# Performance work log

Hardware: AMD Instinct MI355X
Metric: run time of the kernel (lower is better)

## Reference

```python
import jax, jax.numpy as jnp
import numpy as np

B, N_ANG, LX, LY, LZ = 2, 120, 128, 128, 128


def _rotate_z(vol, phi):
    """Rotate vol [B,Lx,Ly,Lz] by phi radians (counterclockwise) in the (x,y)
    plane about the grid center, bilinear interpolation, zero padding.
    Mirrors pytomography's rotate_detector_z (bilinear grid-sample rotate)."""
    Lx, Ly = vol.shape[1], vol.shape[2]
    dt = vol.dtype
    cx = (Lx - 1) / 2.0
    cy = (Ly - 1) / 2.0
    xs = jnp.arange(Lx, dtype=dt) - cx
    ys = jnp.arange(Ly, dtype=dt) - cy
    X, Y = jnp.meshgrid(xs, ys, indexing="ij")  # [Lx,Ly]
    c, s = jnp.cos(phi), jnp.sin(phi)
    # inverse rotation maps each output pixel to its source location
    sx = c * X + s * Y + cx
    sy = -s * X + c * Y + cy
    x0 = jnp.floor(sx)
    y0 = jnp.floor(sy)
    wx = (sx - x0)[None, :, :, None]
    wy = (sy - y0)[None, :, :, None]
    x0i = x0.astype(jnp.int32)
    y0i = y0.astype(jnp.int32)

    def gather(xi, yi):
        valid = (xi >= 0) & (xi < Lx) & (yi >= 0) & (yi < Ly)
        xic = jnp.clip(xi, 0, Lx - 1)
        yic = jnp.clip(yi, 0, Ly - 1)
        v = vol[:, xic, yic, :]  # [B,Lx,Ly,Lz]
        return v * valid.astype(dt)[None, :, :, None]

    v00 = gather(x0i, y0i)
    v01 = gather(x0i, y0i + 1)
    v10 = gather(x0i + 1, y0i)
    v11 = gather(x0i + 1, y0i + 1)
    return (v00 * (1 - wx) * (1 - wy) + v01 * (1 - wx) * wy
            + v10 * wx * (1 - wy) + v11 * wx * wy)


def setup_inputs() -> dict:
    key = jax.random.key(0)
    image = jax.random.uniform(key, (B, N_ANG, LY, LZ), dtype=jnp.float32)
    angles = jnp.linspace(0.0, 360.0, N_ANG, endpoint=False).astype(jnp.float32)
    return {"image": image, "angles": angles}


def reference(image, angles, delta=1e-11):
    # image: [B, N_angles, Lr, Lz]; angles in degrees.
    Bn, Na, Lr, Lz = image.shape
    Lx = Ly = Lr
    dt = image.dtype
    phis = -jnp.deg2rad(angles).astype(dt)  # negative=True -> back-rotation

    def step(carry, inp):
        obj_acc, norm_acc = carry
        proj, phi = inp  # proj: [B, Lr, Lz]
        # image[:, i].unsqueeze(1) * ones([B, Lx, Ly, Lz]): broadcast along x
        obj_i = jnp.broadcast_to(proj[:, None, :, :], (Bn, Lx, Ly, Lz))
        norm_i = jnp.ones((Bn, Lx, Ly, Lz), dt)
        obj_acc = obj_acc + _rotate_z(obj_i, phi)
        norm_acc = norm_acc + _rotate_z(norm_i, phi)
        return (obj_acc, norm_acc), None

    init = (jnp.zeros((Bn, Lx, Ly, Lz), dt), jnp.zeros((Bn, Lx, Ly, Lz), dt))
    (obj, norm), _ = jax.lax.scan(step, init, (jnp.swapaxes(image, 0, 1), phis))
    return obj / (norm + jnp.asarray(delta, dt))
```

## Files before the change

kernel.cpp:

```cpp
#include <hip/hip_runtime.h>

namespace {

constexpr int L     = 128;
constexpr int NANG  = 120;
constexpr size_t H16_BYTES = (size_t)2 * NANG * L * L * 2;

typedef __fp16 f16x2 __attribute__((ext_vector_type(2)));
typedef __fp16 f16x4 __attribute__((ext_vector_type(4)));
typedef float  f32x4 __attribute__((ext_vector_type(4)));

__global__ __launch_bounds__(256) void cvt16_kernel(const float* __restrict__ in,
                                                    unsigned* __restrict__ out) {
    const int i = ((int)blockIdx.x * 256 + (int)threadIdx.x) * 4;
    const float4 v = *reinterpret_cast<const float4*>(in + i);
    f16x2 a = __builtin_amdgcn_cvt_pkrtz(v.x, v.y);
    f16x2 b = __builtin_amdgcn_cvt_pkrtz(v.z, v.w);
    uint2 st;
    st.x = *reinterpret_cast<unsigned*>(&a);
    st.y = *reinterpret_cast<unsigned*>(&b);
    *reinterpret_cast<uint2*>(out + i / 2) = st;
}

template <bool F16>
__global__ __launch_bounds__(1024, 4) void bp_kernel(
    const void* __restrict__ imgv,
    const float* __restrict__ angles,
    float* __restrict__ out)
{
    constexpr unsigned SLICE = F16 ? 32768u : 65536u;
    constexpr unsigned ROWB  = F16 ? 256u  : 512u;
    constexpr int      RSH   = F16 ? 8 : 9;

    __shared__ uint4    wtab[NANG * 64];
    __shared__ float2   acs[NANG];
    __shared__ unsigned arloB[NANG];
    __shared__ alignas(16) float nrmtab[64];

    const int tid = threadIdx.x;
    const int bid = (int)blockIdx.x;
    const int n   = ((bid & 7) << 5) | (bid >> 3);
    int xt = 0, yt = 0;
#pragma unroll
    for (int i = 0; i < 4; ++i) {
        xt |= ((n >> (2 * i)) & 1) << i;
        yt |= ((n >> (2 * i + 1)) & 1) << i;
    }
    const int xb = xt * 8, yb = yt * 8;
    const float cx = (L - 1) * 0.5f;

    if (tid < NANG) {
        const float phi = -angles[tid] * 0.017453292519943295f;
        float s, c;
        sincosf(phi, &s, &c);
        const float X0 = (float)xb - cx,  X1 = (float)(xb + 7) - cx;
        const float Y0 = (float)yb - cx,  Y1 = (float)(yb + 7) - cx;
        const float a00 = -s * X0 + c * Y0 + cx;
        const float a01 = -s * X0 + c * Y1 + cx;
        const float a10 = -s * X1 + c * Y0 + cx;
        const float a11 = -s * X1 + c * Y1 + cx;
        const float symin = fminf(fminf(a00, a01), fminf(a10, a11));
        acs[tid]   = make_float2(c, s);
        arloB[tid] = (unsigned)min(max((int)floorf(symin), 0), 116) << RSH;
    }
    if (tid < 64) nrmtab[tid] = 0.f;
    __syncthreads();

    float wsum = 0.f;
#pragma unroll
    for (int k = 0; k < 8; ++k) {
        const int e = tid + k * 1024;
        if (e < NANG * 64) {
            const int p = e & 63;
            const int a = e >> 6;
            const float2 cs = acs[a];
            const int rlo = (int)(arloB[a] >> RSH);
            const float X = (float)(xb + (p >> 3)) - cx;
            const float Y = (float)(yb + (p & 7)) - cx;
            const float sx =  cs.x * X + cs.y * Y + cx;
            const float sy = -cs.y * X + cs.x * Y + cx;
            const float x0f = floorf(sx), y0f = floorf(sy);
            const float wx = sx - x0f,    wy = sy - y0f;
            const int x0 = (int)x0f, y0 = (int)y0f;
            const float mx0 = (x0 >= 0  && x0 <  L)     ? 1.f : 0.f;
            const float mx1 = (x0 >= -1 && x0 <= L - 2) ? 1.f : 0.f;
            const float my0 = (y0 >= 0  && y0 <  L)     ? 1.f : 0.f;
            const float my1 = (y0 >= -1 && y0 <= L - 2) ? 1.f : 0.f;
            const float A   = (1.f - wx) * mx0 + wx * mx1;
            float w0f = (1.f - wy) * my0 * A;
            float w1f = wy * my1 * A;
            const int y0c = min(max(y0, 0), L - 1);
            const int y1c = min(max(y0 + 1, 0), L - 1);
            const int s0  = min(max(y0c - rlo, 0), 11);
            const int s1  = min(max(y1c - rlo, 0), 11);
            if (s0 == s1) { w0f += w1f; w1f = 0.f; }
            f16x2 wh = __builtin_amdgcn_cvt_pkrtz(w0f, w1f);
            const unsigned wbits = *reinterpret_cast<unsigned*>(&wh);
            const unsigned t  = (unsigned)s0 & 3u;
            const unsigned q0 = (unsigned)s0 >> 2;
            const unsigned long long W = (unsigned long long)wbits << (t * 16u);
            const unsigned spill = (t == 3u) ? (wbits >> 16) : 0u;
            uint4 ent;
            ent.x = (unsigned)W;
            ent.y = (unsigned)(W >> 32);
            ent.z = spill;
            ent.w = q0;
            wtab[a * 64 + p] = ent;
            wsum += w0f + w1f;
        }
    }
    atomicAdd(&nrmtab[tid & 63], wsum);
    __syncthreads();

    const int wave  = tid >> 6;
    const int lane  = tid & 63;
    const int quad  = lane >> 4;
    const int lhalf = lane & 15;
    const int zq    = wave & 3;
    const int b     = (wave >> 2) & 1;
    const int aset  = wave >> 3;
    const char* __restrict__ imgc = (const char*)imgv;

    const unsigned bbase_s = __builtin_amdgcn_readfirstlane((unsigned)(b * NANG) * SLICE);
    const unsigned voffc = (unsigned)((quad == 3) ? 0 : quad) * 4u * ROWB
                         + (unsigned)(zq * 32 + 2 * lhalf) * (F16 ? 2u : 4u);

    f32x4 acc[4][2] = {};

    auto issue = [&](uint4* e, unsigned* r, float2* rf, int i) {
        const int a = aset + 2 * i;
#pragma unroll
        for (int m = 0; m < 4; ++m)
            e[m] = wtab[a * 64 + m * 16 + lhalf];
        const unsigned rlB = __builtin_amdgcn_readfirstlane(arloB[a]);
        const char* pa = imgc + (bbase_s + (unsigned)a * SLICE + rlB);
        if constexpr (F16) {
#pragma unroll
            for (int j = 0; j < 4; ++j)
                r[j] = *(const unsigned*)(pa + (voffc + (unsigned)j * ROWB));
        } else {
#pragma unroll
            for (int j = 0; j < 4; ++j)
                rf[j] = *(const float2*)(pa + (voffc + (unsigned)j * ROWB));
        }
    };
    auto compute = [&](const uint4* e, const unsigned* r, const float2* rf) {
        union { unsigned u[2]; f16x4 v; } B0, B1;
        if constexpr (F16) {
            B0.u[0] = __builtin_amdgcn_perm(r[1], r[0], 0x05040100u);
            B0.u[1] = __builtin_amdgcn_perm(r[3], r[2], 0x05040100u);
            B1.u[0] = __builtin_amdgcn_perm(r[1], r[0], 0x07060302u);
            B1.u[1] = __builtin_amdgcn_perm(r[3], r[2], 0x07060302u);
        } else {
            const f16x2 h0a = __builtin_amdgcn_cvt_pkrtz(rf[0].x, rf[1].x);
            const f16x2 h0b = __builtin_amdgcn_cvt_pkrtz(rf[2].x, rf[3].x);
            const f16x2 h1a = __builtin_amdgcn_cvt_pkrtz(rf[0].y, rf[1].y);
            const f16x2 h1b = __builtin_amdgcn_cvt_pkrtz(rf[2].y, rf[3].y);
            B0.v = f16x4{h0a.x, h0a.y, h0b.x, h0b.y};
            B1.v = f16x4{h1a.x, h1a.y, h1b.x, h1b.y};
        }
#pragma unroll
        for (int m = 0; m < 4; ++m) {
            const int q0 = (int)e[m].w;
            union { unsigned u[2]; f16x4 v; } af;
            af.u[0] = (quad == q0) ? e[m].x : ((quad == q0 + 1) ? e[m].z : 0u);
            af.u[1] = (quad == q0) ? e[m].y : 0u;
            acc[m][0] = __builtin_amdgcn_mfma_f32_16x16x16f16(af.v, B0.v, acc[m][0], 0, 0, 0);
            acc[m][1] = __builtin_amdgcn_mfma_f32_16x16x16f16(af.v, B1.v, acc[m][1], 0, 0, 0);
        }
    };

    uint4    eA[4], eB[4], eC[4];
    unsigned rA[4], rB[4], rC[4];
    float2   fA[4], fB[4], fC[4];

    issue(eA, rA, fA, 0);
    issue(eB, rB, fB, 1);

    for (int i = 0; i < 60; i += 3) {
        if (i + 2 < 60) issue(eC, rC, fC, i + 2);
        compute(eA, rA, fA);
        if (i + 3 < 60) issue(eA, rA, fA, i + 3);
        compute(eB, rB, fB);
        if (i + 4 < 60) issue(eB, rB, fB, i + 4);
        compute(eC, rC, fC);
        __builtin_amdgcn_s_barrier();
    }

    __syncthreads();
    float4* red = reinterpret_cast<float4*>(wtab);
    const int pr = wave & 7;
    if (aset == 1) {
#pragma unroll
        for (int m = 0; m < 4; ++m)
#pragma unroll
            for (int zg = 0; zg < 2; ++zg)
                red[(pr * 8 + m * 2 + zg) * 64 + lane] =
                    make_float4(acc[m][zg][0], acc[m][zg][1],
                                acc[m][zg][2], acc[m][zg][3]);
    }
    __syncthreads();
    if (aset == 0) {
#pragma unroll
        for (int m = 0; m < 4; ++m)
#pragma unroll
            for (int zg = 0; zg < 2; ++zg) {
                const float4 o = red[(pr * 8 + m * 2 + zg) * 64 + lane];
                acc[m][zg][0] += o.x; acc[m][zg][1] += o.y;
                acc[m][zg][2] += o.z; acc[m][zg][3] += o.w;
            }
        const int zb = zq * 32 + 2 * lhalf;
#pragma unroll
        for (int m = 0; m < 4; ++m) {
            const float4 nrm4 = *(const float4*)&nrmtab[m * 16 + quad * 4];
            const float iv[4] = { 1.f / (nrm4.x + 1e-11f), 1.f / (nrm4.y + 1e-11f),
                                  1.f / (nrm4.z + 1e-11f), 1.f / (nrm4.w + 1e-11f) };
#pragma unroll
            for (int r = 0; r < 4; ++r) {
                const int p = m * 16 + quad * 4 + r;
                const int x = xb + (p >> 3);
                const int y = yb + (p & 7);
                const float2 o = make_float2(acc[m][0][r] * iv[r],
                                             acc[m][1][r] * iv[r]);
                *reinterpret_cast<float2*>(
                    &out[(((size_t)(b * L + x)) * L + y) * L + zb]) = o;
            }
        }
    }
}

}

extern "C" void kernel_launch(void* const* d_in, const int* in_sizes, int n_in,
                              void* d_out, int out_size, void* d_ws, size_t ws_size,
                              hipStream_t stream) {
    const float* image  = (const float*)d_in[0];
    const float* angles = (const float*)d_in[1];
    float* out = (float*)d_out;
    (void)in_sizes; (void)n_in; (void)out_size;

    dim3 grid(256);
    if (d_ws != nullptr && ws_size >= H16_BYTES) {
        cvt16_kernel<<<dim3(3840), 256, 0, stream>>>(image, (unsigned*)d_ws);
        bp_kernel<true><<<grid, 1024, 0, stream>>>(d_ws, angles, out);
    } else {
        bp_kernel<false><<<grid, 1024, 0, stream>>>(image, angles, out);
    }
}
```

Baseline: 103.8 us.

## Precompute per-lane MFMA A-fragments in LDS, processed in two angle chunks

The weight table now holds the final per-lane 64-bit f16x4 A operand, with quad selection and spill already applied, so the inner loop no longer needs per-MFMA select logic or 16-byte entries. To fit the larger per-lane table in shared memory, angles are split into two chunks of 60. Each chunk's table is filled, then consumed. This adds an extra fill/sync phase per chunk and moves the norm accumulation to per-element atomics. The pipeline prologue and drain also now happen twice.

```diff
diff --git a/kernel.cpp b/kernel.cpp
--- a/kernel.cpp
+++ b/kernel.cpp
@@ -4,6 +4,7 @@
 
 constexpr int L     = 128;
 constexpr int NANG  = 120;
+constexpr int CHUNK = 60;
 constexpr size_t H16_BYTES = (size_t)2 * NANG * L * L * 2;
 
 typedef __fp16 f16x2 __attribute__((ext_vector_type(2)));
@@ -32,7 +33,7 @@
     constexpr unsigned ROWB  = F16 ? 256u  : 512u;
     constexpr int      RSH   = F16 ? 8 : 9;
 
-    __shared__ uint4    wtab[NANG * 64];
+    __shared__ unsigned long long aftab[CHUNK * 4 * 64];
     __shared__ float2   acs[NANG];
     __shared__ unsigned arloB[NANG];
     __shared__ alignas(16) float nrmtab[64];
@@ -66,13 +67,29 @@
     if (tid < 64) nrmtab[tid] = 0.f;
     __syncthreads();
 
-    float wsum = 0.f;
-#pragma unroll
-    for (int k = 0; k < 8; ++k) {
-        const int e = tid + k * 1024;
-        if (e < NANG * 64) {
-            const int p = e & 63;
-            const int a = e >> 6;
+    const int wave  = tid >> 6;
+    const int lane  = tid & 63;
+    const int quad  = lane >> 4;
+    const int lhalf = lane & 15;
+    const int zq    = wave & 3;
+    const int b     = (wave >> 2) & 1;
+    const int aset  = wave >> 3;
+    const char* __restrict__ imgc = (const char*)imgv;
+
+    const unsigned bbase_s = __builtin_amdgcn_readfirstlane((unsigned)(b * NANG) * SLICE);
+    const unsigned voffc = (unsigned)((quad == 3) ? 0 : quad) * 4u * ROWB
+                         + (unsigned)(zq * 32 + 2 * lhalf) * (F16 ? 2u : 4u);
+
+    auto fill_chunk = [&](int c) {
+#pragma unroll
+        for (int k = 0; k < 15; ++k) {
+            const int e  = tid + k * 1024;
+            const int ln = e & 63;
+            const int m  = (e >> 6) & 3;
+            const int ia = e >> 8;
+            const int a  = c * CHUNK + ia;
+            const int p  = m * 16 + (ln & 15);
+            const int qd = ln >> 4;
             const float2 cs = acs[a];
             const int rlo = (int)(arloB[a] >> RSH);
             const float X = (float)(xb + (p >> 3)) - cx;
@@ -97,41 +114,24 @@
             f16x2 wh = __builtin_amdgcn_cvt_pkrtz(w0f, w1f);
             const unsigned wbits = *reinterpret_cast<unsigned*>(&wh);
             const unsigned t  = (unsigned)s0 & 3u;
-            const unsigned q0 = (unsigned)s0 >> 2;
+            const int      q0 = s0 >> 2;
             const unsigned long long W = (unsigned long long)wbits << (t * 16u);
-            const unsigned spill = (t == 3u) ? (wbits >> 16) : 0u;
-            uint4 ent;
-            ent.x = (unsigned)W;
-            ent.y = (unsigned)(W >> 32);
-            ent.z = spill;
-            ent.w = q0;
-            wtab[a * 64 + p] = ent;
-            wsum += w0f + w1f;
-        }
-    }
-    atomicAdd(&nrmtab[tid & 63], wsum);
-    __syncthreads();
-
-    const int wave  = tid >> 6;
-    const int lane  = tid & 63;
-    const int quad  = lane >> 4;
-    const int lhalf = lane & 15;
-    const int zq    = wave & 3;
-    const int b     = (wave >> 2) & 1;
-    const int aset  = wave >> 3;
-    const char* __restrict__ imgc = (const char*)imgv;
-
-    const unsigned bbase_s = __builtin_amdgcn_readfirstlane((unsigned)(b * NANG) * SLICE);
-    const unsigned voffc = (unsigned)((quad == 3) ? 0 : quad) * 4u * ROWB
-                         + (unsigned)(zq * 32 + 2 * lhalf) * (F16 ? 2u : 4u);
+            const unsigned long long spill =
+                (t == 3u) ? (unsigned long long)(wbits >> 16) : 0ull;
+            aftab[e] = (qd == q0) ? W : ((qd == q0 + 1) ? spill : 0ull);
+            if (qd == 0) atomicAdd(&nrmtab[p], w0f + w1f);
+        }
+    };
 
     f32x4 acc[4][2] = {};
 
-    auto issue = [&](uint4* e, unsigned* r, float2* rf, int i) {
-        const int a = aset + 2 * i;
+    auto issue = [&](unsigned long long* af, unsigned* r, float2* rf,
+                     int i, int c) {
+        const int ia = aset + 2 * i;
+        const int a  = c * CHUNK + ia;
 #pragma unroll
         for (int m = 0; m < 4; ++m)
-            e[m] = wtab[a * 64 + m * 16 + lhalf];
+            af[m] = aftab[ia * 256 + m * 64 + lane];
         const unsigned rlB = __builtin_amdgcn_readfirstlane(arloB[a]);
         const char* pa = imgc + (bbase_s + (unsigned)a * SLICE + rlB);
         if constexpr (F16) {
@@ -144,7 +144,8 @@
                 rf[j] = *(const float2*)(pa + (voffc + (unsigned)j * ROWB));
         }
     };
-    auto compute = [&](const uint4* e, const unsigned* r, const float2* rf) {
+    auto compute = [&](const unsigned long long* af, const unsigned* r,
+                       const float2* rf) {
         union { unsigned u[2]; f16x4 v; } B0, B1;
         if constexpr (F16) {
             B0.u[0] = __builtin_amdgcn_perm(r[1], r[0], 0x05040100u);
@@ -161,34 +162,34 @@
         }
 #pragma unroll
         for (int m = 0; m < 4; ++m) {
-            const int q0 = (int)e[m].w;
-            union { unsigned u[2]; f16x4 v; } af;
-            af.u[0] = (quad == q0) ? e[m].x : ((quad == q0 + 1) ? e[m].z : 0u);
-            af.u[1] = (quad == q0) ? e[m].y : 0u;
-            acc[m][0] = __builtin_amdgcn_mfma_f32_16x16x16f16(af.v, B0.v, acc[m][0], 0, 0, 0);
-            acc[m][1] = __builtin_amdgcn_mfma_f32_16x16x16f16(af.v, B1.v, acc[m][1], 0, 0, 0);
+            union { unsigned long long u; f16x4 v; } afu; afu.u = af[m];
+            acc[m][0] = __builtin_amdgcn_mfma_f32_16x16x16f16(afu.v, B0.v, acc[m][0], 0, 0, 0);
+            acc[m][1] = __builtin_amdgcn_mfma_f32_16x16x16f16(afu.v, B1.v, acc[m][1], 0, 0, 0);
         }
     };
 
-    uint4    eA[4], eB[4], eC[4];
+    unsigned long long aA[4], aB[4], aC[4];
     unsigned rA[4], rB[4], rC[4];
     float2   fA[4], fB[4], fC[4];
 
-    issue(eA, rA, fA, 0);
-    issue(eB, rB, fB, 1);
-
-    for (int i = 0; i < 60; i += 3) {
-        if (i + 2 < 60) issue(eC, rC, fC, i + 2);
-        compute(eA, rA, fA);
-        if (i + 3 < 60) issue(eA, rA, fA, i + 3);
-        compute(eB, rB, fB);
-        if (i + 4 < 60) issue(eB, rB, fB, i + 4);
-        compute(eC, rC, fC);
-        __builtin_amdgcn_s_barrier();
-    }
-
-    __syncthreads();
-    float4* red = reinterpret_cast<float4*>(wtab);
+    for (int c = 0; c < 2; ++c) {
+        fill_chunk(c);
+        __syncthreads();
+        issue(aA, rA, fA, 0, c);
+        issue(aB, rB, fB, 1, c);
+        for (int i = 0; i < 30; i += 3) {
+            if (i + 2 < 30) issue(aC, rC, fC, i + 2, c);
+            compute(aA, rA, fA);
+            if (i + 3 < 30) issue(aA, rA, fA, i + 3, c);
+            compute(aB, rB, fB);
+            if (i + 4 < 30) issue(aB, rB, fB, i + 4, c);
+            compute(aC, rC, fC);
+            __builtin_amdgcn_s_barrier();
+        }
+        __syncthreads();
+    }
+
+    float4* red = reinterpret_cast<float4*>(aftab);
     const int pr = wave & 7;
     if (aset == 1) {
 #pragma unroll
```

Result: slower. 115.0 us (+10.8%).
